# Kernel tuning notes

Hardware: AMD Instinct MI355X
Metric: run time of the kernel (lower is better)

Reference implementation:

```python
import jax, jax.numpy as jnp
import numpy as np

B, LQ, LK, D, NH = 16, 1024, 1024, 160, 8
HD = D // NH
EPS = 1e-5


def _ln(x, g, b):
    m = x.mean(-1, keepdims=True)
    v = ((x - m) ** 2).mean(-1, keepdims=True)
    return (x - m) / jnp.sqrt(v + EPS) * g + b


def _heads(x, L):
    # [B,L,D] -> [B,NH,L,HD]
    return x.reshape(B, L, NH, HD).transpose(0, 2, 1, 3)


def _attn(qh, kh, vh, scale):
    logits = jnp.einsum('bhqd,bhkd->bhqk', qh, kh) * scale
    p = jax.nn.softmax(logits, axis=-1)
    o = jnp.einsum('bhqk,bhkd->bhqd', p, vh)
    return o.transpose(0, 2, 1, 3).reshape(B, -1, D)


def setup_inputs() -> dict:
    key = jax.random.key(0)
    ks = jax.random.split(key, 16)
    s = 0.02
    inp = {
        'q': jax.random.normal(ks[0], (B, LQ, D), jnp.float32),
        'kv': jax.random.normal(ks[1], (B, LK, D), jnp.float32),
        'ln1_g': jnp.ones((D,), jnp.float32), 'ln1_b': jnp.zeros((D,), jnp.float32),
        'sa_in_w': jax.random.normal(ks[2], (3 * D, D), jnp.float32) * s,
        'sa_in_b': jnp.zeros((3 * D,), jnp.float32),
        'sa_out_w': jax.random.normal(ks[3], (D, D), jnp.float32) * s,
        'sa_out_b': jnp.zeros((D,), jnp.float32),
        'ln2_g': jnp.ones((D,), jnp.float32), 'ln2_b': jnp.zeros((D,), jnp.float32),
        'lnkv_g': jnp.ones((D,), jnp.float32), 'lnkv_b': jnp.zeros((D,), jnp.float32),
        'ca_qw': jax.random.normal(ks[4], (D, D), jnp.float32) * s,
        'ca_qb': jnp.zeros((D,), jnp.float32),
        'ca_kw': jax.random.normal(ks[5], (D, D), jnp.float32) * s,
        'ca_kb': jnp.zeros((D,), jnp.float32),
        'ca_vw': jax.random.normal(ks[6], (D, D), jnp.float32) * s,
        'ca_vb': jnp.zeros((D,), jnp.float32),
        'ca_ow': jax.random.normal(ks[7], (D, D), jnp.float32) * s,
        'ca_ob': jnp.zeros((D,), jnp.float32),
        'log_tau': jnp.zeros((1,), jnp.float32),
        'lnf_g': jnp.ones((D,), jnp.float32), 'lnf_b': jnp.zeros((D,), jnp.float32),
        'w1': jax.random.normal(ks[8], (4 * D, D), jnp.float32) * s,
        'b1': jnp.zeros((4 * D,), jnp.float32),
        'w2': jax.random.normal(ks[9], (D, 4 * D), jnp.float32) * s,
        'b2': jnp.zeros((D,), jnp.float32),
    }
    return inp


def reference(q, kv, ln1_g, ln1_b, sa_in_w, sa_in_b, sa_out_w, sa_out_b,
              ln2_g, ln2_b, lnkv_g, lnkv_b, ca_qw, ca_qb, ca_kw, ca_kb,
              ca_vw, ca_vb, ca_ow, ca_ob, log_tau, lnf_g, lnf_b,
              w1, b1, w2, b2):
    # --- self-attention (pre-LN), standard 1/sqrt(hd) scale ---
    qn = _ln(q, ln1_g, ln1_b)
    qkv = qn @ sa_in_w.T + sa_in_b  # [B,LQ,3D]
    sq, sk, sv = jnp.split(qkv, 3, axis=-1)
    sa = _attn(_heads(sq, LQ), _heads(sk, LQ), _heads(sv, LQ), HD ** -0.5)
    sa = sa @ sa_out_w.T + sa_out_b
    q = q + sa  # DropPath is identity in eval

    # --- cross-attention with learnable temperature ---
    qn = _ln(q, ln2_g, ln2_b)
    kvn = _ln(kv, lnkv_g, lnkv_b)
    tau = jnp.minimum(jax.nn.softplus(log_tau) + 0.5, 2.0)  # clamp max=2.0
    scale = (HD ** -0.5) / tau[0]
    qh = _heads(qn @ ca_qw.T + ca_qb, LQ)
    kh = _heads(kvn @ ca_kw.T + ca_kb, LK)
    vh = _heads(kvn @ ca_vw.T + ca_vb, LK)
    ca = _attn(qh, kh, vh, scale) @ ca_ow.T + ca_ob
    q = q + ca

    # --- FFN with exact GELU ---
    h = _ln(q, lnf_g, lnf_b) @ w1.T + b1
    h = jax.nn.gelu(h, approximate=False)
    q = q + (h @ w2.T + b2)
    return q
```

## Files before the change

kernel.cpp:

```cpp
#include <hip/hip_runtime.h>
#include <hip/hip_bf16.h>
#include <math.h>

#define LQN 1024
#define LKN 1024
#define NB 16
#define DM 160
#define NHEADS 8
#define HDIM 20

typedef __attribute__((ext_vector_type(8))) short bf16x8;
typedef __attribute__((ext_vector_type(4))) float f32x4;

__device__ __forceinline__ float bf2f(unsigned short h) {
  union { unsigned int u; float f; } c; c.u = ((unsigned int)h) << 16; return c.f;
}
__device__ __forceinline__ unsigned short f2bf(float f) {
  union { float f; unsigned int u; } c; c.f = f;
  unsigned int lsb = (c.u >> 16) & 1u;
  unsigned int r = c.u + 0x7fffu + lsb;
  return (unsigned short)(r >> 16);
}
__device__ __forceinline__ unsigned int cvtpk(float a, float b) {
  unsigned int r;
  asm("v_cvt_pk_bf16_f32 %0, %1, %2" : "=v"(r) : "v"(a), "v"(b));
  return r;
}
__device__ __forceinline__ float ex2(float x) { return __builtin_amdgcn_exp2f(x); }

__global__ void init_kernel(uint4* __restrict__ zbase, int nz,
                            uint4* __restrict__ vbase, int nv,
                            const float* __restrict__ b0,
                            const float* __restrict__ b1,
                            const float* __restrict__ b2,
                            float* __restrict__ bcat) {
  int i = blockIdx.x * 256 + threadIdx.x;
  if (i < nz) zbase[i] = make_uint4(0, 0, 0, 0);
  if (i < nv) {
    unsigned int v = ((i & 31) == 20) ? 0x3F803F80u : 0u;
    vbase[i] = make_uint4(v, v, v, v);
  }
  if (i < 480) bcat[i] = (i < 160) ? b0[i] : (i < 320 ? b1[i - 160] : b2[i - 320]);
}

struct CvtArgs {
  const float* src[8];
  int cum[9];
};
__global__ void cvt8_kernel(CvtArgs a, unsigned short* __restrict__ dst) {
  int i = blockIdx.x * 256 + threadIdx.x;
  if (i >= 409600) return;
  int s = 0;
#pragma unroll
  for (int t = 0; t < 7; ++t) s += (i >= a.cum[t + 1]) ? 1 : 0;
  dst[i] = f2bf(a.src[s][i - a.cum[s]]);
}

__global__ void ln_kernel(const float* __restrict__ x,
                          const float* __restrict__ g,
                          const float* __restrict__ b,
                          unsigned short* __restrict__ y, int rows) {
  int row = blockIdx.x * 4 + (threadIdx.x >> 6);
  int lane = threadIdx.x & 63;
  const float* xr = x + (size_t)row * DM;
  float a0 = xr[lane];
  float a1 = xr[lane + 64];
  float a2 = (lane < 32) ? xr[lane + 128] : 0.0f;
  float s = a0 + a1 + a2;
#pragma unroll
  for (int m = 1; m < 64; m <<= 1) s += __shfl_xor(s, m);
  float mean = s * (1.0f / DM);
  float d0 = a0 - mean, d1 = a1 - mean, d2 = a2 - mean;
  float vs = d0 * d0 + d1 * d1 + ((lane < 32) ? d2 * d2 : 0.0f);
#pragma unroll
  for (int m = 1; m < 64; m <<= 1) vs += __shfl_xor(vs, m);
  float rstd = rsqrtf(vs * (1.0f / DM) + 1e-5f);
  unsigned short* yr = y + (size_t)row * DM;
  yr[lane]      = f2bf(d0 * rstd * g[lane]      + b[lane]);
  yr[lane + 64] = f2bf(d1 * rstd * g[lane + 64] + b[lane + 64]);
  if (lane < 32)
    yr[lane + 128] = f2bf(d2 * rstd * g[lane + 128] + b[lane + 128]);
}

template <int EPI>
__global__ __launch_bounds__(256, 2)
void gemm160_kernel(const unsigned short* __restrict__ Aq,
                    const unsigned short* __restrict__ Akv,
                    const unsigned short* __restrict__ W,
                    const float* __restrict__ bias,
                    const float* __restrict__ res,
                    void* __restrict__ outp,
                    unsigned short* __restrict__ Kc,
                    unsigned short* __restrict__ Vc) {
  __shared__ unsigned short wl[160 * 168];
  int tid = threadIdx.x;
  int lane = tid & 63;
  int w = tid >> 6;
  int y = blockIdx.y;
  const unsigned short* Wb = W + y * 25600;
#pragma unroll
  for (int p = 0; p < 13; ++p) {
    int idx = p * 2048 + tid * 8;
    if (idx < 25600) {
      int col = idx / 160, k = idx % 160;
      *(uint4*)(wl + col * 168 + k) = *(const uint4*)(Wb + idx);
    }
  }
  __syncthreads();
  int lr = lane & 15;
  int g = lane >> 4;
  int R0 = blockIdx.x * 64;
  int rbase = R0 + w * 16;
  const unsigned short* A = (EPI == 0 && y > 0) ? Akv : Aq;
  const unsigned short* Ap = A + (size_t)(rbase + lr) * 160 + g * 8;
  const unsigned short* wp = wl + lr * 168 + g * 8;
  f32x4 acc[10];
#pragma unroll
  for (int c = 0; c < 10; ++c) acc[c] = (f32x4){0, 0, 0, 0};
#pragma unroll
  for (int k0 = 0; k0 < 160; k0 += 32) {
    bf16x8 a = *(const bf16x8*)(Ap + k0);
#pragma unroll
    for (int c = 0; c < 10; ++c) {
      bf16x8 bfr = *(const bf16x8*)(wp + c * 16 * 168 + k0);
      acc[c] = __builtin_amdgcn_mfma_f32_16x16x32_bf16(a, bfr, acc[c], 0, 0, 0);
    }
  }
  if (EPI == 0) {
    if (y == 0) {
      unsigned short* Qp = (unsigned short*)outp;
#pragma unroll
      for (int c = 0; c < 10; ++c) {
        int col = c * 16 + lr;
        int h = col / 20, d = col % 20;
        float bc = bias[col];
#pragma unroll
        for (int r = 0; r < 4; ++r) {
          int row = rbase + g * 4 + r;
          Qp[(size_t)row * 256 + h * 32 + d] = f2bf(acc[c][r] + bc);
        }
      }
    } else if (y == 1) {
      int b = R0 >> 10;
#pragma unroll
      for (int c = 0; c < 10; ++c) {
        int col = c * 16 + lr;
        int h = col / 20, d = col % 20;
        float bc = bias[160 + col];
        size_t base = ((((size_t)(b * 8 + h)) * 4 + (d >> 3)) * 1024) * 8 + (d & 7);
#pragma unroll
        for (int r = 0; r < 4; ++r) {
          int tok = (rbase + g * 4 + r) & 1023;
          Kc[base + (size_t)tok * 8] = f2bf(acc[c][r] + bc);
        }
      }
    } else {
      int b = R0 >> 10;
      int base64 = R0 & 1023;
      int slotbase = base64 + g * 8 + (w & 1) * 4 + (w >> 1) * 32;
#pragma unroll
      for (int c = 0; c < 10; ++c) {
        int col = c * 16 + lr;
        int h = col / 20, d = col % 20;
        float bc = bias[320 + col];
        size_t vb = ((size_t)(b * 8 + h) * 128) * 256 + (size_t)d * 8;
#pragma unroll
        for (int r = 0; r < 4; ++r) {
          int S = slotbase + r;
          Vc[vb + (size_t)(S >> 3) * 256 + (S & 7)] = f2bf(acc[c][r] + bc);
        }
      }
    }
  } else if (EPI == 1) {
    float* out = (float*)outp;
#pragma unroll
    for (int c = 0; c < 10; ++c) {
      int col = c * 16 + lr;
      float bc = bias[col];
#pragma unroll
      for (int r = 0; r < 4; ++r) {
        int row = rbase + g * 4 + r;
        out[(size_t)row * 160 + col] = acc[c][r] + bc + res[(size_t)row * 160 + col];
      }
    }
  } else {
    unsigned short* out = (unsigned short*)outp;
#pragma unroll
    for (int c = 0; c < 10; ++c) {
      int colg = y * 160 + c * 16 + lr;
      float bc = bias[colg];
#pragma unroll
      for (int r = 0; r < 4; ++r) {
        int row = rbase + g * 4 + r;
        float v = acc[c][r] + bc;
        v = 0.5f * v * (1.0f + erff(v * 0.70710678118654752f));
        out[(size_t)row * 640 + colg] = f2bf(v);
      }
    }
  }
}

template <int K>
__global__ __launch_bounds__(256, 4)
void gemm_kernel(const unsigned short* __restrict__ A,
                 const unsigned short* __restrict__ W,
                 const float* __restrict__ bias,
                 const float* __restrict__ res,
                 float* __restrict__ out, int N) {
  int lane = threadIdx.x & 63;
  int wid = threadIdx.x >> 6;
  int wr = wid >> 1, wc = wid & 1;
  int r0 = blockIdx.x * 64 + wr * 32;
  int c0 = blockIdx.y * 64 + wc * 32;
  if (c0 >= N) return;
  int lr = lane & 15;
  int ko = (lane >> 4) * 8;
  const unsigned short* Ap0 = A + (size_t)(r0 + lr) * K + ko;
  const unsigned short* Ap1 = Ap0 + (size_t)16 * K;
  const unsigned short* Wp0 = W + (size_t)(c0 + lr) * K + ko;
  const unsigned short* Wp1 = Wp0 + (size_t)16 * K;
  f32x4 acc00 = {0, 0, 0, 0}, acc01 = {0, 0, 0, 0};
  f32x4 acc10 = {0, 0, 0, 0}, acc11 = {0, 0, 0, 0};
#pragma unroll
  for (int k = 0; k < K; k += 32) {
    bf16x8 a0 = *(const bf16x8*)(Ap0 + k);
    bf16x8 a1 = *(const bf16x8*)(Ap1 + k);
    bf16x8 b0 = *(const bf16x8*)(Wp0 + k);
    bf16x8 b1 = *(const bf16x8*)(Wp1 + k);
    acc00 = __builtin_amdgcn_mfma_f32_16x16x32_bf16(a0, b0, acc00, 0, 0, 0);
    acc01 = __builtin_amdgcn_mfma_f32_16x16x32_bf16(a0, b1, acc01, 0, 0, 0);
    acc10 = __builtin_amdgcn_mfma_f32_16x16x32_bf16(a1, b0, acc10, 0, 0, 0);
    acc11 = __builtin_amdgcn_mfma_f32_16x16x32_bf16(a1, b1, acc11, 0, 0, 0);
  }
  int cA = c0 + lr, cB = c0 + 16 + lr;
  float bc0 = bias[cA];
  float bc1 = bias[cB];
  int rb = (lane >> 4) * 4;
#pragma unroll
  for (int i = 0; i < 2; ++i) {
    f32x4 aA = i ? acc10 : acc00;
    f32x4 aB = i ? acc11 : acc01;
#pragma unroll
    for (int r = 0; r < 4; ++r) {
      int row = r0 + i * 16 + rb + r;
      out[(size_t)row * N + cA] = aA[r] + bc0 + res[(size_t)row * N + cA];
      out[(size_t)row * N + cB] = aB[r] + bc1 + res[(size_t)row * N + cB];
    }
  }
}

__global__ __launch_bounds__(256, 4)
void attn_kernel(const unsigned short* __restrict__ Qp,
                 const unsigned short* __restrict__ Kc,
                 const unsigned short* __restrict__ Vc,
                 unsigned short* __restrict__ O,
                 const float* __restrict__ tau_ptr,
                 float base_scale) {
  __shared__ unsigned short kbuf[2][2048];
  __shared__ unsigned short vbuf[2][2048];
  int lane = threadIdx.x & 63;
  int wid = threadIdx.x >> 6;
  int bh = blockIdx.x;
  int b = bh >> 3, h = bh & 7;
  int q0 = blockIdx.y * 128 + wid * 32;
  float sc = base_scale;
  if (tau_ptr) {
    float lt = tau_ptr[0];
    float sp = (lt > 20.0f) ? lt : log1pf(expf(lt));
    sc /= fminf(sp + 0.5f, 2.0f);
  }
  float scale = sc * 1.4426950408889634f;
  int lr = lane & 15;
  int g = lane >> 4;
  int ko = g * 8;
  int rb = g * 4;
  const size_t tb = (size_t)b * LQN;
  union { bf16x8 v; unsigned short s[8]; unsigned int u[4]; } fq0, fq1;
  fq0.v = *(const bf16x8*)(Qp + (tb + q0 + lr) * 256 + h * 32 + ko);
  fq1.v = *(const bf16x8*)(Qp + (tb + q0 + 16 + lr) * 256 + h * 32 + ko);
#pragma unroll
  for (int j = 0; j < 4; ++j) {
    fq0.u[j] = cvtpk(bf2f(fq0.s[2 * j]) * scale, bf2f(fq0.s[2 * j + 1]) * scale);
    fq1.u[j] = cvtpk(bf2f(fq1.s[2 * j]) * scale, bf2f(fq1.s[2 * j + 1]) * scale);
  }
  bf16x8 aq0 = fq0.v, aq1 = fq1.v;
  const unsigned short* ksrc = Kc + (((size_t)bh * 4 + wid) * 1024) * 8;
  const unsigned short* vsrc = Vc + (size_t)bh * 32768;
  int sdst = wid * 512 + lane * 8;
  {
    uint4 k0 = *(const uint4*)(ksrc + lane * 8);
    uint4 v0 = *(const uint4*)(vsrc + sdst);
    *(uint4*)(kbuf[0] + sdst) = k0;
    *(uint4*)(vbuf[0] + sdst) = v0;
  }
  __syncthreads();
  int cur = 0;
  f32x4 o00 = {0, 0, 0, 0}, o01 = {0, 0, 0, 0};
  f32x4 o10 = {0, 0, 0, 0}, o11 = {0, 0, 0, 0};
  const f32x4 zero = {0, 0, 0, 0};
  for (int kt = 0; kt < LKN; kt += 64) {
    int ktn = (kt + 64 < LKN) ? kt + 64 : 0;
    uint4 kn = *(const uint4*)(ksrc + (ktn + lane) * 8);
    uint4 vn = *(const uint4*)(vsrc + ktn * 32 + sdst);
    const unsigned short* kb = kbuf[cur];
    const unsigned short* vbp = vbuf[cur];
    bf16x8 ck0 = *(const bf16x8*)(kb + g * 512 + lr * 8);
    bf16x8 ck1 = *(const bf16x8*)(kb + g * 512 + (16 + lr) * 8);
    bf16x8 ck2 = *(const bf16x8*)(kb + g * 512 + (32 + lr) * 8);
    bf16x8 ck3 = *(const bf16x8*)(kb + g * 512 + (48 + lr) * 8);
    f32x4 s0 = __builtin_amdgcn_mfma_f32_16x16x32_bf16(ck0, aq0, zero, 0, 0, 0);
    f32x4 s1 = __builtin_amdgcn_mfma_f32_16x16x32_bf16(ck1, aq0, zero, 0, 0, 0);
    f32x4 s2 = __builtin_amdgcn_mfma_f32_16x16x32_bf16(ck2, aq0, zero, 0, 0, 0);
    f32x4 s3 = __builtin_amdgcn_mfma_f32_16x16x32_bf16(ck3, aq0, zero, 0, 0, 0);
    union { bf16x8 v; unsigned int u[4]; } palo1, palo2, pahi1, pahi2;
    palo1.u[0] = cvtpk(ex2(s0[0]), ex2(s0[1]));
    palo1.u[1] = cvtpk(ex2(s0[2]), ex2(s0[3]));
    palo1.u[2] = cvtpk(ex2(s1[0]), ex2(s1[1]));
    palo1.u[3] = cvtpk(ex2(s1[2]), ex2(s1[3]));
    palo2.u[0] = cvtpk(ex2(s2[0]), ex2(s2[1]));
    palo2.u[1] = cvtpk(ex2(s2[2]), ex2(s2[3]));
    palo2.u[2] = cvtpk(ex2(s3[0]), ex2(s3[1]));
    palo2.u[3] = cvtpk(ex2(s3[2]), ex2(s3[3]));
    s0 = __builtin_amdgcn_mfma_f32_16x16x32_bf16(ck0, aq1, zero, 0, 0, 0);
    s1 = __builtin_amdgcn_mfma_f32_16x16x32_bf16(ck1, aq1, zero, 0, 0, 0);
    s2 = __builtin_amdgcn_mfma_f32_16x16x32_bf16(ck2, aq1, zero, 0, 0, 0);
    s3 = __builtin_amdgcn_mfma_f32_16x16x32_bf16(ck3, aq1, zero, 0, 0, 0);
    pahi1.u[0] = cvtpk(ex2(s0[0]), ex2(s0[1]));
    pahi1.u[1] = cvtpk(ex2(s0[2]), ex2(s0[3]));
    pahi1.u[2] = cvtpk(ex2(s1[0]), ex2(s1[1]));
    pahi1.u[3] = cvtpk(ex2(s1[2]), ex2(s1[3]));
    pahi2.u[0] = cvtpk(ex2(s2[0]), ex2(s2[1]));
    pahi2.u[1] = cvtpk(ex2(s2[2]), ex2(s2[3]));
    pahi2.u[2] = cvtpk(ex2(s3[0]), ex2(s3[1]));
    pahi2.u[3] = cvtpk(ex2(s3[2]), ex2(s3[3]));
    bf16x8 vb00 = *(const bf16x8*)(vbp + g * 256 + lr * 8);
    bf16x8 vb01 = *(const bf16x8*)(vbp + (4 + g) * 256 + lr * 8);
    bf16x8 vb10 = *(const bf16x8*)(vbp + g * 256 + (16 + lr) * 8);
    bf16x8 vb11 = *(const bf16x8*)(vbp + (4 + g) * 256 + (16 + lr) * 8);
    o00 = __builtin_amdgcn_mfma_f32_16x16x32_bf16(palo1.v, vb00, o00, 0, 0, 0);
    o00 = __builtin_amdgcn_mfma_f32_16x16x32_bf16(palo2.v, vb01, o00, 0, 0, 0);
    o01 = __builtin_amdgcn_mfma_f32_16x16x32_bf16(palo1.v, vb10, o01, 0, 0, 0);
    o01 = __builtin_amdgcn_mfma_f32_16x16x32_bf16(palo2.v, vb11, o01, 0, 0, 0);
    o10 = __builtin_amdgcn_mfma_f32_16x16x32_bf16(pahi1.v, vb00, o10, 0, 0, 0);
    o10 = __builtin_amdgcn_mfma_f32_16x16x32_bf16(pahi2.v, vb01, o10, 0, 0, 0);
    o11 = __builtin_amdgcn_mfma_f32_16x16x32_bf16(pahi1.v, vb10, o11, 0, 0, 0);
    o11 = __builtin_amdgcn_mfma_f32_16x16x32_bf16(pahi2.v, vb11, o11, 0, 0, 0);
    *(uint4*)(kbuf[cur ^ 1] + sdst) = kn;
    *(uint4*)(vbuf[cur ^ 1] + sdst) = vn;
    __syncthreads();
    cur ^= 1;
  }
  unsigned short* ob = O + (tb + q0) * DM + h * HDIM;
  int psl = (lane & 48) + 4;
#pragma unroll
  for (int r = 0; r < 4; ++r) {
    int qr = rb + r;
    float inv0 = 1.0f / __shfl(o01[r], psl, 64);
    ob[(size_t)qr * DM + lr] = f2bf(o00[r] * inv0);
    if (lr < 4) ob[(size_t)qr * DM + 16 + lr] = f2bf(o01[r] * inv0);
    float inv1 = 1.0f / __shfl(o11[r], psl, 64);
    ob[(size_t)(16 + qr) * DM + lr] = f2bf(o10[r] * inv1);
    if (lr < 4) ob[(size_t)(16 + qr) * DM + 16 + lr] = f2bf(o11[r] * inv1);
  }
}

extern "C" void kernel_launch(void* const* d_in, const int* in_sizes, int n_in,
                              void* d_out, int out_size, void* d_ws, size_t ws_size,
                              hipStream_t stream) {
  (void)in_sizes; (void)n_in; (void)out_size; (void)ws_size;
  const float* q        = (const float*)d_in[0];
  const float* kv       = (const float*)d_in[1];
  const float* ln1_g    = (const float*)d_in[2];
  const float* ln1_b    = (const float*)d_in[3];
  const float* sa_in_w  = (const float*)d_in[4];
  const float* sa_in_b  = (const float*)d_in[5];
  const float* sa_out_w = (const float*)d_in[6];
  const float* sa_out_b = (const float*)d_in[7];
  const float* ln2_g    = (const float*)d_in[8];
  const float* ln2_b    = (const float*)d_in[9];
  const float* lnkv_g   = (const float*)d_in[10];
  const float* lnkv_b   = (const float*)d_in[11];
  const float* ca_qw    = (const float*)d_in[12];
  const float* ca_qb    = (const float*)d_in[13];
  const float* ca_kw    = (const float*)d_in[14];
  const float* ca_kb    = (const float*)d_in[15];
  const float* ca_vw    = (const float*)d_in[16];
  const float* ca_vb    = (const float*)d_in[17];
  const float* ca_ow    = (const float*)d_in[18];
  const float* ca_ob    = (const float*)d_in[19];
  const float* log_tau  = (const float*)d_in[20];
  const float* lnf_g    = (const float*)d_in[21];
  const float* lnf_b    = (const float*)d_in[22];
  const float* w1       = (const float*)d_in[23];
  const float* b1       = (const float*)d_in[24];
  const float* w2       = (const float*)d_in[25];
  const float* b2       = (const float*)d_in[26];

  const int M = NB * LQN;
  char* ws = (char*)d_ws;
  unsigned short* wb   = (unsigned short*)(ws);
  float*          bcat = (float*)(ws + 860160);
  unsigned short* qn   = (unsigned short*)(ws + 1048576);
  unsigned short* sqp  = (unsigned short*)(ws + 6291456);
  unsigned short* skc  = (unsigned short*)(ws + 14680064);
  unsigned short* svc  = (unsigned short*)(ws + 23068672);
  unsigned short* attn = (unsigned short*)(ws + 31457280);
  unsigned short* kvn  = (unsigned short*)(ws + 36700160);
  float*          q1   = (float*)(ws + 41943040);
  float*          q2   = (float*)(ws + 52428800);
  unsigned short* hbuf = (unsigned short*)(ws + 6291456);

  unsigned short* b_sa_in  = wb;
  unsigned short* b_sa_out = wb + 76800;
  unsigned short* b_ca_q   = wb + 102400;
  unsigned short* b_ca_o   = wb + 179200;
  unsigned short* b_w1     = wb + 204800;
  unsigned short* b_w2     = wb + 307200;

  dim3 blk(256);
  const float isq = 0.22360679774997896f;

  init_kernel<<<dim3(4096), blk, 0, stream>>>(
      (uint4*)(ws + 6291456), 1048576, (uint4*)(ws + 23068672), 524288,
      ca_qb, ca_kb, ca_vb, bcat);

  CvtArgs ca;
  ca.src[0] = sa_in_w;  ca.src[1] = sa_out_w; ca.src[2] = ca_qw; ca.src[3] = ca_kw;
  ca.src[4] = ca_vw;    ca.src[5] = ca_ow;    ca.src[6] = w1;    ca.src[7] = w2;
  int cum[9] = {0, 76800, 102400, 128000, 153600, 179200, 204800, 307200, 409600};
  for (int i = 0; i < 9; ++i) ca.cum[i] = cum[i];
  cvt8_kernel<<<dim3(1600), blk, 0, stream>>>(ca, wb);

  ln_kernel<<<dim3(M / 4), blk, 0, stream>>>(q, ln1_g, ln1_b, qn, M);
  gemm160_kernel<0><<<dim3(M / 64, 3), blk, 0, stream>>>(
      qn, qn, b_sa_in, sa_in_b, nullptr, sqp, skc, svc);
  attn_kernel<<<dim3(NB * NHEADS, LQN / 128), blk, 0, stream>>>(sqp, skc, svc, attn, nullptr, isq);
  gemm160_kernel<1><<<dim3(M / 64, 1), blk, 0, stream>>>(
      attn, attn, b_sa_out, sa_out_b, q, q1, nullptr, nullptr);

  ln_kernel<<<dim3(M / 4), blk, 0, stream>>>(q1, ln2_g, ln2_b, qn, M);
  ln_kernel<<<dim3(M / 4), blk, 0, stream>>>(kv, lnkv_g, lnkv_b, kvn, M);
  gemm160_kernel<0><<<dim3(M / 64, 3), blk, 0, stream>>>(
      qn, kvn, b_ca_q, bcat, nullptr, sqp, skc, svc);
  attn_kernel<<<dim3(NB * NHEADS, LQN / 128), blk, 0, stream>>>(sqp, skc, svc, attn, log_tau, isq);
  gemm160_kernel<1><<<dim3(M / 64, 1), blk, 0, stream>>>(
      attn, attn, b_ca_o, ca_ob, q1, q2, nullptr, nullptr);

  ln_kernel<<<dim3(M / 4), blk, 0, stream>>>(q2, lnf_g, lnf_b, qn, M);
  gemm160_kernel<2><<<dim3(M / 64, 4), blk, 0, stream>>>(
      qn, qn, b_w1, b1, nullptr, hbuf, nullptr, nullptr);
  gemm_kernel<640><<<dim3(M / 64, 3), blk, 0, stream>>>(hbuf, b_w2, b2, q2, (float*)d_out, 160);
}
```

Baseline: 175.8 us.

## Fuse setup and LN kernels, split out-proj GEMM columns, double attention KV tile

Merges the weight bf16 conversion into the init kernel and the two cross-attention LayerNorms into one launch, which cuts launch count. The output-projection GEMMs are split into two column halves so the grid has twice as many blocks. The attention kernel now stages 128 keys per iteration instead of 64, halving barrier count, at the cost of twice the LDS per block. Each of these is a separate idea aimed at launch overhead, occupancy and sync cost.

After: 171.6 us. 1.02x faster.

```diff
diff --git a/kernel.cpp b/kernel.cpp
--- a/kernel.cpp
+++ b/kernel.cpp
@@ -28,12 +28,18 @@
 }
 __device__ __forceinline__ float ex2(float x) { return __builtin_amdgcn_exp2f(x); }
 
+struct CvtArgs {
+  const float* src[8];
+  int cum[9];
+};
+
 __global__ void init_kernel(uint4* __restrict__ zbase, int nz,
                             uint4* __restrict__ vbase, int nv,
                             const float* __restrict__ b0,
                             const float* __restrict__ b1,
                             const float* __restrict__ b2,
-                            float* __restrict__ bcat) {
+                            float* __restrict__ bcat,
+                            CvtArgs a, unsigned short* __restrict__ wdst) {
   int i = blockIdx.x * 256 + threadIdx.x;
   if (i < nz) zbase[i] = make_uint4(0, 0, 0, 0);
   if (i < nv) {
@@ -41,19 +47,12 @@
     vbase[i] = make_uint4(v, v, v, v);
   }
   if (i < 480) bcat[i] = (i < 160) ? b0[i] : (i < 320 ? b1[i - 160] : b2[i - 320]);
-}
-
-struct CvtArgs {
-  const float* src[8];
-  int cum[9];
-};
-__global__ void cvt8_kernel(CvtArgs a, unsigned short* __restrict__ dst) {
-  int i = blockIdx.x * 256 + threadIdx.x;
-  if (i >= 409600) return;
-  int s = 0;
-#pragma unroll
-  for (int t = 0; t < 7; ++t) s += (i >= a.cum[t + 1]) ? 1 : 0;
-  dst[i] = f2bf(a.src[s][i - a.cum[s]]);
+  if (i < 409600) {
+    int s = 0;
+#pragma unroll
+    for (int t = 0; t < 7; ++t) s += (i >= a.cum[t + 1]) ? 1 : 0;
+    wdst[i] = f2bf(a.src[s][i - a.cum[s]]);
+  }
 }
 
 __global__ void ln_kernel(const float* __restrict__ x,
@@ -82,7 +81,42 @@
     yr[lane + 128] = f2bf(d2 * rstd * g[lane + 128] + b[lane + 128]);
 }
 
-template <int EPI>
+__global__ void ln2_kernel(const float* __restrict__ x1,
+                           const float* __restrict__ g1,
+                           const float* __restrict__ b1,
+                           unsigned short* __restrict__ y1,
+                           const float* __restrict__ x2,
+                           const float* __restrict__ g2,
+                           const float* __restrict__ b2,
+                           unsigned short* __restrict__ y2, int rowsPer) {
+  int row = blockIdx.x * 4 + (threadIdx.x >> 6);
+  int lane = threadIdx.x & 63;
+  const float* x; const float* g; const float* b; unsigned short* y;
+  if (row < rowsPer) {
+    x = x1 + (size_t)row * DM; g = g1; b = b1; y = y1 + (size_t)row * DM;
+  } else {
+    int r2 = row - rowsPer;
+    x = x2 + (size_t)r2 * DM; g = g2; b = b2; y = y2 + (size_t)r2 * DM;
+  }
+  float a0 = x[lane];
+  float a1 = x[lane + 64];
+  float a2 = (lane < 32) ? x[lane + 128] : 0.0f;
+  float s = a0 + a1 + a2;
+#pragma unroll
+  for (int m = 1; m < 64; m <<= 1) s += __shfl_xor(s, m);
+  float mean = s * (1.0f / DM);
+  float d0 = a0 - mean, d1 = a1 - mean, d2 = a2 - mean;
+  float vs = d0 * d0 + d1 * d1 + ((lane < 32) ? d2 * d2 : 0.0f);
+#pragma unroll
+  for (int m = 1; m < 64; m <<= 1) vs += __shfl_xor(vs, m);
+  float rstd = rsqrtf(vs * (1.0f / DM) + 1e-5f);
+  y[lane]      = f2bf(d0 * rstd * g[lane]      + b[lane]);
+  y[lane + 64] = f2bf(d1 * rstd * g[lane + 64] + b[lane + 64]);
+  if (lane < 32)
+    y[lane + 128] = f2bf(d2 * rstd * g[lane + 128] + b[lane + 128]);
+}
+
+template <int EPI, int NCOL>
 __global__ __launch_bounds__(256, 2)
 void gemm160_kernel(const unsigned short* __restrict__ Aq,
                     const unsigned short* __restrict__ Akv,
@@ -92,19 +126,15 @@
                     void* __restrict__ outp,
                     unsigned short* __restrict__ Kc,
                     unsigned short* __restrict__ Vc) {
-  __shared__ unsigned short wl[160 * 168];
+  __shared__ unsigned short wl[NCOL * 16 * 168];
   int tid = threadIdx.x;
   int lane = tid & 63;
   int w = tid >> 6;
   int y = blockIdx.y;
-  const unsigned short* Wb = W + y * 25600;
-#pragma unroll
-  for (int p = 0; p < 13; ++p) {
-    int idx = p * 2048 + tid * 8;
-    if (idx < 25600) {
-      int col = idx / 160, k = idx % 160;
-      *(uint4*)(wl + col * 168 + k) = *(const uint4*)(Wb + idx);
-    }
+  const unsigned short* Wb = W + y * (NCOL * 2560);
+  for (int idx = tid * 8; idx < NCOL * 2560; idx += 2048) {
+    int col = idx / 160, k = idx % 160;
+    *(uint4*)(wl + col * 168 + k) = *(const uint4*)(Wb + idx);
   }
   __syncthreads();
   int lr = lane & 15;
@@ -114,14 +144,14 @@
   const unsigned short* A = (EPI == 0 && y > 0) ? Akv : Aq;
   const unsigned short* Ap = A + (size_t)(rbase + lr) * 160 + g * 8;
   const unsigned short* wp = wl + lr * 168 + g * 8;
-  f32x4 acc[10];
-#pragma unroll
-  for (int c = 0; c < 10; ++c) acc[c] = (f32x4){0, 0, 0, 0};
+  f32x4 acc[NCOL];
+#pragma unroll
+  for (int c = 0; c < NCOL; ++c) acc[c] = (f32x4){0, 0, 0, 0};
 #pragma unroll
   for (int k0 = 0; k0 < 160; k0 += 32) {
     bf16x8 a = *(const bf16x8*)(Ap + k0);
 #pragma unroll
-    for (int c = 0; c < 10; ++c) {
+    for (int c = 0; c < NCOL; ++c) {
       bf16x8 bfr = *(const bf16x8*)(wp + c * 16 * 168 + k0);
       acc[c] = __builtin_amdgcn_mfma_f32_16x16x32_bf16(a, bfr, acc[c], 0, 0, 0);
     }
@@ -130,7 +160,7 @@
     if (y == 0) {
       unsigned short* Qp = (unsigned short*)outp;
 #pragma unroll
-      for (int c = 0; c < 10; ++c) {
+      for (int c = 0; c < NCOL; ++c) {
         int col = c * 16 + lr;
         int h = col / 20, d = col % 20;
         float bc = bias[col];
@@ -143,7 +173,7 @@
     } else if (y == 1) {
       int b = R0 >> 10;
 #pragma unroll
-      for (int c = 0; c < 10; ++c) {
+      for (int c = 0; c < NCOL; ++c) {
         int col = c * 16 + lr;
         int h = col / 20, d = col % 20;
         float bc = bias[160 + col];
@@ -159,7 +189,7 @@
       int base64 = R0 & 1023;
       int slotbase = base64 + g * 8 + (w & 1) * 4 + (w >> 1) * 32;
 #pragma unroll
-      for (int c = 0; c < 10; ++c) {
+      for (int c = 0; c < NCOL; ++c) {
         int col = c * 16 + lr;
         int h = col / 20, d = col % 20;
         float bc = bias[320 + col];
@@ -174,20 +204,20 @@
   } else if (EPI == 1) {
     float* out = (float*)outp;
 #pragma unroll
-    for (int c = 0; c < 10; ++c) {
-      int col = c * 16 + lr;
-      float bc = bias[col];
+    for (int c = 0; c < NCOL; ++c) {
+      int gcol = y * NCOL * 16 + c * 16 + lr;
+      float bc = bias[gcol];
 #pragma unroll
       for (int r = 0; r < 4; ++r) {
         int row = rbase + g * 4 + r;
-        out[(size_t)row * 160 + col] = acc[c][r] + bc + res[(size_t)row * 160 + col];
+        out[(size_t)row * 160 + gcol] = acc[c][r] + bc + res[(size_t)row * 160 + gcol];
       }
     }
   } else {
     unsigned short* out = (unsigned short*)outp;
 #pragma unroll
-    for (int c = 0; c < 10; ++c) {
-      int colg = y * 160 + c * 16 + lr;
+    for (int c = 0; c < NCOL; ++c) {
+      int colg = y * NCOL * 16 + c * 16 + lr;
       float bc = bias[colg];
 #pragma unroll
       for (int r = 0; r < 4; ++r) {
@@ -256,8 +286,8 @@
                  unsigned short* __restrict__ O,
                  const float* __restrict__ tau_ptr,
                  float base_scale) {
-  __shared__ unsigned short kbuf[2][2048];
-  __shared__ unsigned short vbuf[2][2048];
+  __shared__ unsigned short kbuf[2][4096];
+  __shared__ unsigned short vbuf[2][4096];
   int lane = threadIdx.x & 63;
   int wid = threadIdx.x >> 6;
   int bh = blockIdx.x;
@@ -286,70 +316,87 @@
   bf16x8 aq0 = fq0.v, aq1 = fq1.v;
   const unsigned short* ksrc = Kc + (((size_t)bh * 4 + wid) * 1024) * 8;
   const unsigned short* vsrc = Vc + (size_t)bh * 32768;
-  int sdst = wid * 512 + lane * 8;
+  int sd = wid * 1024 + lane * 8;
   {
     uint4 k0 = *(const uint4*)(ksrc + lane * 8);
-    uint4 v0 = *(const uint4*)(vsrc + sdst);
-    *(uint4*)(kbuf[0] + sdst) = k0;
-    *(uint4*)(vbuf[0] + sdst) = v0;
+    uint4 k1 = *(const uint4*)(ksrc + (64 + lane) * 8);
+    uint4 v0 = *(const uint4*)(vsrc + sd);
+    uint4 v1 = *(const uint4*)(vsrc + sd + 512);
+    *(uint4*)(kbuf[0] + sd) = k0;
+    *(uint4*)(kbuf[0] + sd + 512) = k1;
+    *(uint4*)(vbuf[0] + sd) = v0;
+    *(uint4*)(vbuf[0] + sd + 512) = v1;
   }
   __syncthreads();
   int cur = 0;
   f32x4 o00 = {0, 0, 0, 0}, o01 = {0, 0, 0, 0};
   f32x4 o10 = {0, 0, 0, 0}, o11 = {0, 0, 0, 0};
   const f32x4 zero = {0, 0, 0, 0};
-  for (int kt = 0; kt < LKN; kt += 64) {
-    int ktn = (kt + 64 < LKN) ? kt + 64 : 0;
-    uint4 kn = *(const uint4*)(ksrc + (ktn + lane) * 8);
-    uint4 vn = *(const uint4*)(vsrc + ktn * 32 + sdst);
-    const unsigned short* kb = kbuf[cur];
-    const unsigned short* vbp = vbuf[cur];
-    bf16x8 ck0 = *(const bf16x8*)(kb + g * 512 + lr * 8);
-    bf16x8 ck1 = *(const bf16x8*)(kb + g * 512 + (16 + lr) * 8);
-    bf16x8 ck2 = *(const bf16x8*)(kb + g * 512 + (32 + lr) * 8);
-    bf16x8 ck3 = *(const bf16x8*)(kb + g * 512 + (48 + lr) * 8);
-    f32x4 s0 = __builtin_amdgcn_mfma_f32_16x16x32_bf16(ck0, aq0, zero, 0, 0, 0);
-    f32x4 s1 = __builtin_amdgcn_mfma_f32_16x16x32_bf16(ck1, aq0, zero, 0, 0, 0);
-    f32x4 s2 = __builtin_amdgcn_mfma_f32_16x16x32_bf16(ck2, aq0, zero, 0, 0, 0);
-    f32x4 s3 = __builtin_amdgcn_mfma_f32_16x16x32_bf16(ck3, aq0, zero, 0, 0, 0);
-    union { bf16x8 v; unsigned int u[4]; } palo1, palo2, pahi1, pahi2;
-    palo1.u[0] = cvtpk(ex2(s0[0]), ex2(s0[1]));
-    palo1.u[1] = cvtpk(ex2(s0[2]), ex2(s0[3]));
-    palo1.u[2] = cvtpk(ex2(s1[0]), ex2(s1[1]));
-    palo1.u[3] = cvtpk(ex2(s1[2]), ex2(s1[3]));
-    palo2.u[0] = cvtpk(ex2(s2[0]), ex2(s2[1]));
-    palo2.u[1] = cvtpk(ex2(s2[2]), ex2(s2[3]));
-    palo2.u[2] = cvtpk(ex2(s3[0]), ex2(s3[1]));
-    palo2.u[3] = cvtpk(ex2(s3[2]), ex2(s3[3]));
-    s0 = __builtin_amdgcn_mfma_f32_16x16x32_bf16(ck0, aq1, zero, 0, 0, 0);
-    s1 = __builtin_amdgcn_mfma_f32_16x16x32_bf16(ck1, aq1, zero, 0, 0, 0);
-    s2 = __builtin_amdgcn_mfma_f32_16x16x32_bf16(ck2, aq1, zero, 0, 0, 0);
-    s3 = __builtin_amdgcn_mfma_f32_16x16x32_bf16(ck3, aq1, zero, 0, 0, 0);
-    pahi1.u[0] = cvtpk(ex2(s0[0]), ex2(s0[1]));
-    pahi1.u[1] = cvtpk(ex2(s0[2]), ex2(s0[3]));
-    pahi1.u[2] = cvtpk(ex2(s1[0]), ex2(s1[1]));
-    pahi1.u[3] = cvtpk(ex2(s1[2]), ex2(s1[3]));
-    pahi2.u[0] = cvtpk(ex2(s2[0]), ex2(s2[1]));
-    pahi2.u[1] = cvtpk(ex2(s2[2]), ex2(s2[3]));
-    pahi2.u[2] = cvtpk(ex2(s3[0]), ex2(s3[1]));
-    pahi2.u[3] = cvtpk(ex2(s3[2]), ex2(s3[3]));
-    bf16x8 vb00 = *(const bf16x8*)(vbp + g * 256 + lr * 8);
-    bf16x8 vb01 = *(const bf16x8*)(vbp + (4 + g) * 256 + lr * 8);
-    bf16x8 vb10 = *(const bf16x8*)(vbp + g * 256 + (16 + lr) * 8);
-    bf16x8 vb11 = *(const bf16x8*)(vbp + (4 + g) * 256 + (16 + lr) * 8);
-    o00 = __builtin_amdgcn_mfma_f32_16x16x32_bf16(palo1.v, vb00, o00, 0, 0, 0);
-    o00 = __builtin_amdgcn_mfma_f32_16x16x32_bf16(palo2.v, vb01, o00, 0, 0, 0);
-    o01 = __builtin_amdgcn_mfma_f32_16x16x32_bf16(palo1.v, vb10, o01, 0, 0, 0);
-    o01 = __builtin_amdgcn_mfma_f32_16x16x32_bf16(palo2.v, vb11, o01, 0, 0, 0);
-    o10 = __builtin_amdgcn_mfma_f32_16x16x32_bf16(pahi1.v, vb00, o10, 0, 0, 0);
-    o10 = __builtin_amdgcn_mfma_f32_16x16x32_bf16(pahi2.v, vb01, o10, 0, 0, 0);
-    o11 = __builtin_amdgcn_mfma_f32_16x16x32_bf16(pahi1.v, vb10, o11, 0, 0, 0);
-    o11 = __builtin_amdgcn_mfma_f32_16x16x32_bf16(pahi2.v, vb11, o11, 0, 0, 0);
-    *(uint4*)(kbuf[cur ^ 1] + sdst) = kn;
-    *(uint4*)(vbuf[cur ^ 1] + sdst) = vn;
+
+#define ATTN_COMPUTE(KB, VB)                                                   \
+  {                                                                            \
+    const unsigned short* kp_ = (KB);                                          \
+    const unsigned short* vp_ = (VB);                                          \
+    bf16x8 ck0 = *(const bf16x8*)(kp_ + g * 1024 + lr * 8);                    \
+    bf16x8 ck1 = *(const bf16x8*)(kp_ + g * 1024 + (16 + lr) * 8);             \
+    bf16x8 ck2 = *(const bf16x8*)(kp_ + g * 1024 + (32 + lr) * 8);             \
+    bf16x8 ck3 = *(const bf16x8*)(kp_ + g * 1024 + (48 + lr) * 8);             \
+    f32x4 s0 = __builtin_amdgcn_mfma_f32_16x16x32_bf16(ck0, aq0, zero, 0, 0, 0);\
+    f32x4 s1 = __builtin_amdgcn_mfma_f32_16x16x32_bf16(ck1, aq0, zero, 0, 0, 0);\
+    f32x4 s2 = __builtin_amdgcn_mfma_f32_16x16x32_bf16(ck2, aq0, zero, 0, 0, 0);\
+    f32x4 s3 = __builtin_amdgcn_mfma_f32_16x16x32_bf16(ck3, aq0, zero, 0, 0, 0);\
+    union { bf16x8 v; unsigned int u[4]; } p1, p2, p3, p4;                     \
+    p1.u[0] = cvtpk(ex2(s0[0]), ex2(s0[1]));                                   \
+    p1.u[1] = cvtpk(ex2(s0[2]), ex2(s0[3]));                                   \
+    p1.u[2] = cvtpk(ex2(s1[0]), ex2(s1[1]));                                   \
+    p1.u[3] = cvtpk(ex2(s1[2]), ex2(s1[3]));                                   \
+    p2.u[0] = cvtpk(ex2(s2[0]), ex2(s2[1]));                                   \
+    p2.u[1] = cvtpk(ex2(s2[2]), ex2(s2[3]));                                   \
+    p2.u[2] = cvtpk(ex2(s3[0]), ex2(s3[1]));                                   \
+    p2.u[3] = cvtpk(ex2(s3[2]), ex2(s3[3]));                                   \
+    s0 = __builtin_amdgcn_mfma_f32_16x16x32_bf16(ck0, aq1, zero, 0, 0, 0);     \
+    s1 = __builtin_amdgcn_mfma_f32_16x16x32_bf16(ck1, aq1, zero, 0, 0, 0);     \
+    s2 = __builtin_amdgcn_mfma_f32_16x16x32_bf16(ck2, aq1, zero, 0, 0, 0);     \
+    s3 = __builtin_amdgcn_mfma_f32_16x16x32_bf16(ck3, aq1, zero, 0, 0, 0);     \
+    p3.u[0] = cvtpk(ex2(s0[0]), ex2(s0[1]));                                   \
+    p3.u[1] = cvtpk(ex2(s0[2]), ex2(s0[3]));                                   \
+    p3.u[2] = cvtpk(ex2(s1[0]), ex2(s1[1]));                                   \
+    p3.u[3] = cvtpk(ex2(s1[2]), ex2(s1[3]));                                   \
+    p4.u[0] = cvtpk(ex2(s2[0]), ex2(s2[1]));                                   \
+    p4.u[1] = cvtpk(ex2(s2[2]), ex2(s2[3]));                                   \
+    p4.u[2] = cvtpk(ex2(s3[0]), ex2(s3[1]));                                   \
+    p4.u[3] = cvtpk(ex2(s3[2]), ex2(s3[3]));                                   \
+    bf16x8 w00 = *(const bf16x8*)(vp_ + g * 256 + lr * 8);                     \
+    bf16x8 w01 = *(const bf16x8*)(vp_ + (4 + g) * 256 + lr * 8);               \
+    bf16x8 w10 = *(const bf16x8*)(vp_ + g * 256 + (16 + lr) * 8);              \
+    bf16x8 w11 = *(const bf16x8*)(vp_ + (4 + g) * 256 + (16 + lr) * 8);        \
+    o00 = __builtin_amdgcn_mfma_f32_16x16x32_bf16(p1.v, w00, o00, 0, 0, 0);    \
+    o00 = __builtin_amdgcn_mfma_f32_16x16x32_bf16(p2.v, w01, o00, 0, 0, 0);    \
+    o01 = __builtin_amdgcn_mfma_f32_16x16x32_bf16(p1.v, w10, o01, 0, 0, 0);    \
+    o01 = __builtin_amdgcn_mfma_f32_16x16x32_bf16(p2.v, w11, o01, 0, 0, 0);    \
+    o10 = __builtin_amdgcn_mfma_f32_16x16x32_bf16(p3.v, w00, o10, 0, 0, 0);    \
+    o10 = __builtin_amdgcn_mfma_f32_16x16x32_bf16(p4.v, w01, o10, 0, 0, 0);    \
+    o11 = __builtin_amdgcn_mfma_f32_16x16x32_bf16(p3.v, w10, o11, 0, 0, 0);    \
+    o11 = __builtin_amdgcn_mfma_f32_16x16x32_bf16(p4.v, w11, o11, 0, 0, 0);    \
+  }
+
+#pragma unroll 1
+  for (int kt = 0; kt < LKN; kt += 128) {
+    int ktn = (kt + 128 < LKN) ? kt + 128 : 0;
+    uint4 kA0 = *(const uint4*)(ksrc + (ktn + lane) * 8);
+    uint4 kA1 = *(const uint4*)(ksrc + (ktn + 64 + lane) * 8);
+    uint4 vA0 = *(const uint4*)(vsrc + ktn * 32 + sd);
+    uint4 vA1 = *(const uint4*)(vsrc + ktn * 32 + sd + 512);
+    ATTN_COMPUTE(kbuf[cur], vbuf[cur])
+    *(uint4*)(kbuf[cur ^ 1] + sd) = kA0;
+    *(uint4*)(kbuf[cur ^ 1] + sd + 512) = kA1;
+    ATTN_COMPUTE(kbuf[cur] + 512, vbuf[cur] + 2048)
+    *(uint4*)(vbuf[cur ^ 1] + sd) = vA0;
+    *(uint4*)(vbuf[cur ^ 1] + sd + 512) = vA1;
     __syncthreads();
     cur ^= 1;
   }
+#undef ATTN_COMPUTE
   unsigned short* ob = O + (tb + q0) * DM + h * HDIM;
   int psl = (lane & 48) + 4;
 #pragma unroll
@@ -420,34 +467,32 @@
   dim3 blk(256);
   const float isq = 0.22360679774997896f;
 
-  init_kernel<<<dim3(4096), blk, 0, stream>>>(
-      (uint4*)(ws + 6291456), 1048576, (uint4*)(ws + 23068672), 524288,
-      ca_qb, ca_kb, ca_vb, bcat);
-
   CvtArgs ca;
   ca.src[0] = sa_in_w;  ca.src[1] = sa_out_w; ca.src[2] = ca_qw; ca.src[3] = ca_kw;
   ca.src[4] = ca_vw;    ca.src[5] = ca_ow;    ca.src[6] = w1;    ca.src[7] = w2;
   int cum[9] = {0, 76800, 102400, 128000, 153600, 179200, 204800, 307200, 409600};
   for (int i = 0; i < 9; ++i) ca.cum[i] = cum[i];
-  cvt8_kernel<<<dim3(1600), blk, 0, stream>>>(ca, wb);
+  init_kernel<<<dim3(4096), blk, 0, stream>>>(
+      (uint4*)(ws + 6291456), 1048576, (uint4*)(ws + 23068672), 524288,
+      ca_qb, ca_kb, ca_vb, bcat, ca, wb);
 
   ln_kernel<<<dim3(M / 4), blk, 0, stream>>>(q, ln1_g, ln1_b, qn, M);
-  gemm160_kernel<0><<<dim3(M / 64, 3), blk, 0, stream>>>(
+  gemm160_kernel<0, 10><<<dim3(M / 64, 3), blk, 0, stream>>>(
       qn, qn, b_sa_in, sa_in_b, nullptr, sqp, skc, svc);
   attn_kernel<<<dim3(NB * NHEADS, LQN / 128), blk, 0, stream>>>(sqp, skc, svc, attn, nullptr, isq);
-  gemm160_kernel<1><<<dim3(M / 64, 1), blk, 0, stream>>>(
+  gemm160_kernel<1, 5><<<dim3(M / 64, 2), blk, 0, stream>>>(
       attn, attn, b_sa_out, sa_out_b, q, q1, nullptr, nullptr);
 
-  ln_kernel<<<dim3(M / 4), blk, 0, stream>>>(q1, ln2_g, ln2_b, qn, M);
-  ln_kernel<<<dim3(M / 4), blk, 0, stream>>>(kv, lnkv_g, lnkv_b, kvn, M);
-  gemm160_kernel<0><<<dim3(M / 64, 3), blk, 0, stream>>>(
+  ln2_kernel<<<dim3(M / 2), blk, 0, stream>>>(q1, ln2_g, ln2_b, qn,
+                                              kv, lnkv_g, lnkv_b, kvn, M);
+  gemm160_kernel<0, 10><<<dim3(M / 64, 3), blk, 0, stream>>>(
       qn, kvn, b_ca_q, bcat, nullptr, sqp, skc, svc);
   attn_kernel<<<dim3(NB * NHEADS, LQN / 128), blk, 0, stream>>>(sqp, skc, svc, attn, log_tau, isq);
-  gemm160_kernel<1><<<dim3(M / 64, 1), blk, 0, stream>>>(
+  gemm160_kernel<1, 5><<<dim3(M / 64, 2), blk, 0, stream>>>(
       attn, attn, b_ca_o, ca_ob, q1, q2, nullptr, nullptr);
 
   ln_kernel<<<dim3(M / 4), blk, 0, stream>>>(q2, lnf_g, lnf_b, qn, M);
-  gemm160_kernel<2><<<dim3(M / 64, 4), blk, 0, stream>>>(
+  gemm160_kernel<2, 10><<<dim3(M / 64, 4), blk, 0, stream>>>(
       qn, qn, b_w1, b1, nullptr, hbuf, nullptr, nullptr);
   gemm_kernel<640><<<dim3(M / 64, 3), blk, 0, stream>>>(hbuf, b_w2, b2, q2, (float*)d_out, 160);
 }
```
